# Kernel optimization log

Measured on AMD Instinct MI355X. Metric: run time of the kernel, lower is better.

The kernel has to match this reference:

```python
import jax, jax.numpy as jnp
import numpy as np

B, Q, C = 8, 100, 1024
H, W = 64, 64
NH = 16
HD = C // NH
SCALE = HD ** -0.5
LN_EPS = 1e-5


def setup_inputs() -> dict:
    key = jax.random.key(0)
    ks = jax.random.split(key, 8)
    xav = lambda k, shp: jax.random.normal(k, shp, jnp.float32) * (2.0 / (shp[0] + shp[-1])) ** 0.5
    return {
        "tgt": jax.random.normal(ks[0], (B, Q, C), jnp.float32),
        "memory": jax.random.normal(ks[1], (B, H, W, C), jnp.float32),
        "memory_pos_emb": jax.random.normal(ks[2], (B, H, W, C), jnp.float32),
        "query_pos_emb": jax.random.normal(ks[3], (B, Q, C), jnp.float32),
        "Wq": xav(ks[4], (C, C)),
        "Wk": xav(ks[5], (C, C)),
        "Wv": xav(ks[6], (C, C)),
        "Wo": xav(ks[7], (C, C)),
        "bo": jnp.zeros((C,), jnp.float32),
        "ln_gamma": jnp.ones((C,), jnp.float32),
        "ln_beta": jnp.zeros((C,), jnp.float32),
    }


def _layernorm(x, g, b):
    mu = jnp.mean(x, axis=-1, keepdims=True)
    var = jnp.var(x, axis=-1, keepdims=True)
    return (x - mu) * jax.lax.rsqrt(var + LN_EPS) * g + b


def reference(tgt, memory, memory_pos_emb, query_pos_emb, Wq, Wk, Wv, Wo, bo, ln_gamma, ln_beta):
    # flatten spatial dims: [B,H,W,C] -> [B,K,C]
    mem = memory.reshape(B, H * W, C)
    mpos = memory_pos_emb.reshape(B, H * W, C)
    q_in = tgt + query_pos_emb          # [B,Q,C]
    k_in = mem + mpos                    # [B,K,C]
    # projections (torch Linear: x @ W.T), split heads -> [B,nh,*,hd]
    q = (q_in @ Wq.T).reshape(B, Q, NH, HD).transpose(0, 2, 1, 3)
    k = (k_in @ Wk.T).reshape(B, -1, NH, HD).transpose(0, 2, 1, 3)
    v = (mem @ Wv.T).reshape(B, -1, NH, HD).transpose(0, 2, 1, 3)
    dots = jnp.einsum('bhid,bhjd->bhij', q, k) * SCALE   # [B,nh,Q,K]
    # slot attention: softmax over QUERY axis, then renormalize over keys
    attn = jax.nn.softmax(dots, axis=2)
    attn = attn / (jnp.sum(attn, axis=-1, keepdims=True) + 1e-8)
    updates = jnp.einsum('bhij,bhjd->bhid', attn, v)     # [B,nh,Q,hd]
    updates = updates.transpose(0, 2, 1, 3).reshape(B, Q, C)
    out = updates @ Wo.T + bo
    # residual (dropout is identity in eval) + post-LayerNorm
    return _layernorm(tgt + out, ln_gamma, ln_beta)
```

## Files before the change

### kernel.cpp

```cpp
#include <hip/hip_runtime.h>

typedef unsigned short u16;
typedef __attribute__((ext_vector_type(8))) short bf16x8;
typedef __attribute__((ext_vector_type(4))) short bf16x4;
typedef __attribute__((ext_vector_type(4))) float f32x4;
typedef __attribute__((ext_vector_type(4))) unsigned short u16x4;
typedef __attribute__((ext_vector_type(8))) unsigned short u16x8;
typedef __attribute__((ext_vector_type(4))) int i32x4;
typedef __attribute__((ext_vector_type(4))) float f4;

#define DI __device__ __forceinline__


DI u16 f2bf(float f){
  unsigned int u = __float_as_uint(f);
  return (u16)((u + 0x7FFFu + ((u >> 16) & 1u)) >> 16);
}

DI void gl_lds16(const void* g, void* l){
  __builtin_amdgcn_global_load_lds((const __attribute__((address_space(1))) unsigned int*)g,
                                   (__attribute__((address_space(3))) unsigned int*)l, 16, 0, 0);
}

__global__ __launch_bounds__(256) void prep_kv(const float* __restrict__ mem,
                                               const float* __restrict__ mpos,
                                               u16* __restrict__ kA, u16* __restrict__ vA){
  const int t = blockIdx.x * 256 + threadIdx.x;
  #pragma unroll
  for (int i = 0; i < 2; ++i){
    const size_t g = (size_t)t + (size_t)i * 2097152;
    f4 m0 = ((const f4*)mem)[g * 2];
    f4 m1 = ((const f4*)mem)[g * 2 + 1];
    f4 p0 = ((const f4*)mpos)[g * 2];
    f4 p1 = ((const f4*)mpos)[g * 2 + 1];
    u16x8 k, v;
    #pragma unroll
    for (int j = 0; j < 4; ++j){
      k[j]     = f2bf(m0[j] + p0[j]);  v[j]     = f2bf(m0[j]);
      k[j + 4] = f2bf(m1[j] + p1[j]);  v[j + 4] = f2bf(m1[j]);
    }
    ((u16x8*)kA)[g] = k;
    ((u16x8*)vA)[g] = v;
  }
}

__global__ __launch_bounds__(256) void prep_qw(const float* __restrict__ tgt,
                                               const float* __restrict__ qpos,
                                               const float* __restrict__ Wq, const float* __restrict__ Wk,
                                               const float* __restrict__ Wv, const float* __restrict__ Wo,
                                               u16* __restrict__ qA, u16* __restrict__ Wbf){
  int gid = blockIdx.x * 256 + threadIdx.x;
  const int NQ4 = 819200 / 4;
  if (gid < NQ4){
    f4 a = ((const f4*)tgt)[gid];
    f4 b = ((const f4*)qpos)[gid];
    u16x4 r;
    #pragma unroll
    for (int j = 0; j < 4; ++j) r[j] = f2bf(a[j] + b[j]);
    ((u16x4*)qA)[gid] = r;
  } else {
    int wid = gid - NQ4;
    int sel = wid >> 18;
    int off = wid & 262143;
    const float* W = (sel == 0) ? Wq : (sel == 1) ? Wk : (sel == 2) ? Wv : Wo;
    f4 w = ((const f4*)W)[off];
    u16x4 r;
    #pragma unroll
    for (int j = 0; j < 4; ++j) r[j] = f2bf(w[j]);
    ((u16x4*)(Wbf))[(size_t)sel * 262144 + off] = r;
  }
}

__global__ __launch_bounds__(512, 1) void gemm256(
    const u16* __restrict__ A, const u16* __restrict__ Bw,
    u16* __restrict__ Cb, float scale)
{
  __shared__ __align__(16) char lds[131072];
  const int tid = threadIdx.x;
  const int l = tid & 63, w = tid >> 6;
  const int nwg = gridDim.x;
  const int sbid = (blockIdx.x & 7) * (nwg >> 3) + (blockIdx.x >> 3);
  const int mb = sbid >> 2, nb = sbid & 3;
  const int m0 = mb * 256, n0 = nb * 256;
  const int fr = l & 15, fg = l >> 4;
  const int wm = w >> 2, wn = w & 3;

  char* ldsA  = lds + wm * 8192 + l * 16;
  char* ldsB  = lds + 32768 + wn * 4096 + l * 16;
  char* ldsS0 = lds + w * 1024;
  char* ldsS1 = lds + (8 + w) * 1024;
  const u16* gA0 = A  + (size_t)(m0 + w * 16 + fr) * 1024 + fg * 8;
  const u16* gA1 = A  + (size_t)(m0 + (8 + w) * 16 + fr) * 1024 + fg * 8;
  const u16* gB0 = Bw + (size_t)(n0 + w * 16 + fr) * 1024 + fg * 8;
  const u16* gB1 = Bw + (size_t)(n0 + (8 + w) * 16 + fr) * 1024 + fg * 8;

  auto stA = [&](int pp, int kh, int kt){
    const int o = kt * 64 + kh * 32;
    gl_lds16(gA0 + o, ldsS0 + pp * 65536 + kh * 16384);
    gl_lds16(gA1 + o, ldsS1 + pp * 65536 + kh * 16384);
  };
  auto stB = [&](int pp, int kh, int kt){
    const int o = kt * 64 + kh * 32;
    gl_lds16(gB0 + o, ldsS0 + pp * 65536 + 32768 + kh * 16384);
    gl_lds16(gB1 + o, ldsS1 + pp * 65536 + 32768 + kh * 16384);
  };
  auto rdA4 = [&](bf16x8* av, int pp, int kh, int mfb){
    #pragma unroll
    for (int i = 0; i < 4; ++i)
      av[i] = *(const bf16x8*)(ldsA + pp * 65536 + kh * 16384 + (mfb + i) * 1024);
  };
  auto rdB4 = [&](bf16x8* bv, int pp, int kh){
    #pragma unroll
    for (int i = 0; i < 4; ++i)
      bv[i] = *(const bf16x8*)(ldsB + pp * 65536 + kh * 16384 + i * 1024);
  };

  f32x4 acc[8][4] = {};

  stA(0, 0, 0); stB(0, 0, 0); stA(0, 1, 0); stB(0, 1, 0);
  stA(1, 0, 1); stB(1, 0, 1);
  asm volatile("s_waitcnt vmcnt(8)" ::: "memory");
  __builtin_amdgcn_s_barrier();

  auto ktbody = [&](int P, int kt){
    const int kt1 = (kt + 1 > 15) ? 15 : kt + 1;
    const int kt2 = (kt + 2 > 15) ? 15 : kt + 2;
    bf16x8 av[4], bv[4];

    rdA4(av, P, 0, 0); rdB4(bv, P, 0);
    stA(P ^ 1, 1, kt1);
    __builtin_amdgcn_s_barrier();
    __builtin_amdgcn_s_setprio(1);
    #pragma unroll
    for (int i = 0; i < 4; ++i)
      #pragma unroll
      for (int n = 0; n < 4; ++n)
        acc[i][n] = __builtin_amdgcn_mfma_f32_16x16x32_bf16(av[i], bv[n], acc[i][n], 0, 0, 0);
    __builtin_amdgcn_s_setprio(0);
    __builtin_amdgcn_s_barrier();

    rdA4(av, P, 0, 4);
    stB(P ^ 1, 1, kt1);
    asm volatile("s_waitcnt vmcnt(8)" ::: "memory");
    __builtin_amdgcn_s_barrier();
    __builtin_amdgcn_s_setprio(1);
    #pragma unroll
    for (int i = 0; i < 4; ++i)
      #pragma unroll
      for (int n = 0; n < 4; ++n)
        acc[4 + i][n] = __builtin_amdgcn_mfma_f32_16x16x32_bf16(av[i], bv[n], acc[4 + i][n], 0, 0, 0);
    __builtin_amdgcn_s_setprio(0);
    __builtin_amdgcn_s_barrier();

    rdA4(av, P, 1, 0); rdB4(bv, P, 1);
    stA(P, 0, kt2);
    __builtin_amdgcn_s_barrier();
    __builtin_amdgcn_s_setprio(1);
    #pragma unroll
    for (int i = 0; i < 4; ++i)
      #pragma unroll
      for (int n = 0; n < 4; ++n)
        acc[i][n] = __builtin_amdgcn_mfma_f32_16x16x32_bf16(av[i], bv[n], acc[i][n], 0, 0, 0);
    __builtin_amdgcn_s_setprio(0);
    __builtin_amdgcn_s_barrier();

    rdA4(av, P, 1, 4);
    stB(P, 0, kt2);
    asm volatile("s_waitcnt vmcnt(8)" ::: "memory");
    __builtin_amdgcn_s_barrier();
    __builtin_amdgcn_s_setprio(1);
    #pragma unroll
    for (int i = 0; i < 4; ++i)
      #pragma unroll
      for (int n = 0; n < 4; ++n)
        acc[4 + i][n] = __builtin_amdgcn_mfma_f32_16x16x32_bf16(av[i], bv[n], acc[4 + i][n], 0, 0, 0);
    __builtin_amdgcn_s_setprio(0);
    __builtin_amdgcn_s_barrier();
  };

  for (int kk = 0; kk < 8; ++kk){
    ktbody(0, 2 * kk);
    ktbody(1, 2 * kk + 1);
  }

  asm volatile("s_waitcnt vmcnt(0)" ::: "memory");

  #pragma unroll
  for (int mf = 0; mf < 8; ++mf){
    #pragma unroll
    for (int nf = 0; nf < 4; ++nf){
      const int gcol = n0 + wn * 64 + nf * 16 + fr;
      #pragma unroll
      for (int r = 0; r < 4; ++r){
        const int grow = m0 + wm * 128 + mf * 16 + fg * 4 + r;
        Cb[(size_t)grow * 1024 + gcol] = f2bf(acc[mf][nf][r] * scale);
      }
    }
  }
}

template<int MODE>
__global__ __launch_bounds__(256, 2) void gemm_bt(
    const u16* __restrict__ A, const u16* __restrict__ Bw,
    u16* __restrict__ Cb, float* __restrict__ Cf,
    const float* __restrict__ bias, const float* __restrict__ resid,
    int M, float scale)
{
  __shared__ u16 lA[2][128 * 32];
  __shared__ u16 lB[2][128 * 32];
  const int tid = threadIdx.x;
  const int l = tid & 63, w = tid >> 6;
  const int nwg = gridDim.x;
  int bid = blockIdx.x;
  bid = (bid & 7) * (nwg >> 3) + (bid >> 3);
  const int mb = bid >> 3, nb = bid & 7;
  const int m0 = mb * 128, n0 = nb * 128;
  const int fr = l & 15, fg = l >> 4;
  const int wr = w >> 1, wc = w & 1;

  f32x4 acc[4][4] = {};

  auto stage = [&](int buf, int kt){
    const int k0 = kt * 32;
    #pragma unroll
    for (int q = 0; q < 2; ++q){
      int r = w * 32 + q * 16 + (l >> 2);
      int ar = m0 + r; if (ar >= M) ar = M - 1;
      gl_lds16(A  + (size_t)ar * 1024 + k0 + (l & 3) * 8, &lA[buf][(w * 32 + q * 16) * 32]);
      gl_lds16(Bw + (size_t)(n0 + r) * 1024 + k0 + (l & 3) * 8, &lB[buf][(w * 32 + q * 16) * 32]);
    }
  };

  stage(0, 0);
  __syncthreads();
  for (int kt = 0; kt < 32; ++kt){
    const int cur = kt & 1;
    if (kt < 31) stage(cur ^ 1, kt + 1);
    bf16x8 av[4], bv[4];
    #pragma unroll
    for (int m = 0; m < 4; ++m)
      av[m] = *(const bf16x8*)&lA[cur][(wr * 64 + m * 16 + fr) * 32 + fg * 8];
    #pragma unroll
    for (int n = 0; n < 4; ++n)
      bv[n] = *(const bf16x8*)&lB[cur][(wc * 64 + n * 16 + fr) * 32 + fg * 8];
    #pragma unroll
    for (int m = 0; m < 4; ++m)
      #pragma unroll
      for (int n = 0; n < 4; ++n)
        acc[m][n] = __builtin_amdgcn_mfma_f32_16x16x32_bf16(av[m], bv[n], acc[m][n], 0, 0, 0);
    __syncthreads();
  }

  #pragma unroll
  for (int m = 0; m < 4; ++m){
    const int grow_base = m0 + wr * 64 + m * 16 + fg * 4;
    #pragma unroll
    for (int n = 0; n < 4; ++n){
      const int gcol = n0 + wc * 64 + n * 16 + fr;
      #pragma unroll
      for (int r = 0; r < 4; ++r){
        const int grow = grow_base + r;
        if (grow < M){
          const float v = acc[m][n][r];
          if (MODE == 0) Cb[(size_t)grow * 1024 + gcol] = f2bf(v * scale);
          else           Cf[(size_t)grow * 1024 + gcol] = v + bias[gcol] + resid[(size_t)grow * 1024 + gcol];
        }
      }
    }
  }
}

__global__ __launch_bounds__(64, 1) void attn_k(
    const u16* __restrict__ qp, const u16* __restrict__ kp, const u16* __restrict__ vp,
    float* __restrict__ updpart, float* __restrict__ rspart)
{
  const int bidx = blockIdx.x;
  const int c = bidx & 7, h = (bidx >> 3) & 15, b = bidx >> 7;
  const int bh = b * 16 + h;
  const int l = threadIdx.x;
  const int fr = l & 15, fg = l >> 4;

  __shared__ u16 qlds[112 * 64];
  for (int t = 0; t < 14; ++t){
    int chunk = t * 64 + l;
    int row = chunk >> 3, cb = chunk & 7;
    i32x4 val = {0, 0, 0, 0};
    if (row < 100)
      val = *(const i32x4*)(qp + (size_t)(b * 100 + row) * 1024 + h * 64 + cb * 8);
    *(i32x4*)((char*)qlds + row * 128 + ((cb ^ (row & 7)) * 16)) = val;
  }
  __syncthreads();

  bf16x8 qf[7][2];
  #pragma unroll
  for (int n = 0; n < 7; ++n)
    #pragma unroll
    for (int ks = 0; ks < 2; ++ks){
      int row = n * 16 + fr;
      int cb = ks * 4 + fg;
      qf[n][ks] = *(const bf16x8*)((const char*)qlds + row * 128 + ((cb ^ (row & 7)) * 16));
    }

  f32x4 acc[7][4] = {};
  float rs[7] = {};
  const f32x4 fz = {0.f, 0.f, 0.f, 0.f};
  const size_t kvbase = ((size_t)b * 4096) * 1024 + h * 64;

  for (int t = 0; t < 32; ++t){
    const int j0 = c * 512 + t * 16;
    bf16x8 kf0 = *(const bf16x8*)(kp + kvbase + (size_t)(j0 + fr) * 1024 + fg * 8);
    bf16x8 kf1 = *(const bf16x8*)(kp + kvbase + (size_t)(j0 + fr) * 1024 + 32 + fg * 8);
    f32x4 s[7];
    #pragma unroll
    for (int n = 0; n < 7; ++n){
      s[n] = __builtin_amdgcn_mfma_f32_16x16x32_bf16(kf0, qf[n][0], fz, 0, 0, 0);
      s[n] = __builtin_amdgcn_mfma_f32_16x16x32_bf16(kf1, qf[n][1], s[n], 0, 0, 0);
    }
    if (fr >= 4){ s[6][0] = -1e30f; s[6][1] = -1e30f; s[6][2] = -1e30f; s[6][3] = -1e30f; }

    float pv[7][4];
    #pragma unroll
    for (int r = 0; r < 4; ++r){
      float m = s[0][r];
      #pragma unroll
      for (int n = 1; n < 7; ++n) m = fmaxf(m, s[n][r]);
      m = fmaxf(m, __shfl_xor(m, 1)); m = fmaxf(m, __shfl_xor(m, 2));
      m = fmaxf(m, __shfl_xor(m, 4)); m = fmaxf(m, __shfl_xor(m, 8));
      float sum = 0.f;
      #pragma unroll
      for (int n = 0; n < 7; ++n){ float e = __expf(s[n][r] - m); pv[n][r] = e; sum += e; }
      sum += __shfl_xor(sum, 1); sum += __shfl_xor(sum, 2);
      sum += __shfl_xor(sum, 4); sum += __shfl_xor(sum, 8);
      float inv = 1.0f / sum;
      #pragma unroll
      for (int n = 0; n < 7; ++n) pv[n][r] *= inv;
    }

    bf16x4 pk[7];
    #pragma unroll
    for (int n = 0; n < 7; ++n){
      rs[n] += pv[n][0] + pv[n][1] + pv[n][2] + pv[n][3];
      bf16x4 t4;
      t4[0] = (short)f2bf(pv[n][0]); t4[1] = (short)f2bf(pv[n][1]);
      t4[2] = (short)f2bf(pv[n][2]); t4[3] = (short)f2bf(pv[n][3]);
      pk[n] = t4;
    }

    bf16x4 vf[4];
    #pragma unroll
    for (int dt = 0; dt < 4; ++dt){
      bf16x4 tv;
      #pragma unroll
      for (int jj = 0; jj < 4; ++jj)
        tv[jj] = (short)vp[kvbase + (size_t)(j0 + fg * 4 + jj) * 1024 + dt * 16 + fr];
      vf[dt] = tv;
    }

    #pragma unroll
    for (int n = 0; n < 7; ++n)
      #pragma unroll
      for (int dt = 0; dt < 4; ++dt)
        acc[n][dt] = __builtin_amdgcn_mfma_f32_16x16x16bf16_1k(vf[dt], pk[n], acc[n][dt], 0, 0, 0);
  }

  #pragma unroll
  for (int n = 0; n < 7; ++n){
    float v = rs[n];
    v += __shfl_xor(v, 16); v += __shfl_xor(v, 32);
    if (l < 16) rspart[((size_t)c * 128 + bh) * 112 + n * 16 + l] = v;
  }
  float* ub = updpart + ((size_t)c * 128 + bh) * 64 * 112;
  #pragma unroll
  for (int n = 0; n < 7; ++n)
    #pragma unroll
    for (int dt = 0; dt < 4; ++dt)
      #pragma unroll
      for (int r = 0; r < 4; ++r){
        int d = dt * 16 + fg * 4 + r;
        int i = n * 16 + fr;
        ub[d * 112 + i] = acc[n][dt][r];
      }
}

__global__ __launch_bounds__(256) void nrm_k(const float* __restrict__ updpart,
                                             const float* __restrict__ rspart,
                                             u16* __restrict__ updn){
  int gid = blockIdx.x * 256 + threadIdx.x;
  int b = gid / 102400;
  int rem = gid % 102400;
  int i = rem / 1024;
  int cc = rem & 1023;
  int h = cc >> 6, d = cc & 63;
  int bh = b * 16 + h;
  float sum = 0.f, rsum = 0.f;
  #pragma unroll
  for (int c = 0; c < 8; ++c){
    sum  += updpart[(((size_t)c * 128 + bh) * 64 + d) * 112 + i];
    rsum += rspart[((size_t)c * 128 + bh) * 112 + i];
  }
  updn[gid] = f2bf(sum / (rsum + 1e-8f));
}

__global__ __launch_bounds__(256) void ln_k(const float* __restrict__ x,
                                            const float* __restrict__ g,
                                            const float* __restrict__ be,
                                            float* __restrict__ out){
  const int row = blockIdx.x;
  const int tid = threadIdx.x;
  const f4 xv = *(const f4*)(x + (size_t)row * 1024 + tid * 4);
  float s = xv[0] + xv[1] + xv[2] + xv[3];
  float q = xv[0]*xv[0] + xv[1]*xv[1] + xv[2]*xv[2] + xv[3]*xv[3];
  #pragma unroll
  for (int m = 1; m < 64; m <<= 1){ s += __shfl_xor(s, m); q += __shfl_xor(q, m); }
  __shared__ float ss[4], qq[4];
  const int w = tid >> 6;
  if ((tid & 63) == 0){ ss[w] = s; qq[w] = q; }
  __syncthreads();
  s = ss[0] + ss[1] + ss[2] + ss[3];
  q = qq[0] + qq[1] + qq[2] + qq[3];
  const float mu = s * (1.0f / 1024.0f);
  const float var = q * (1.0f / 1024.0f) - mu * mu;
  const float rstd = rsqrtf(var + 1e-5f);
  const f4 gv = *(const f4*)(g + tid * 4);
  const f4 bv = *(const f4*)(be + tid * 4);
  f4 o;
  #pragma unroll
  for (int j = 0; j < 4; ++j) o[j] = (xv[j] - mu) * rstd * gv[j] + bv[j];
  *(f4*)(out + (size_t)row * 1024 + tid * 4) = o;
}

extern "C" void kernel_launch(void* const* d_in, const int* in_sizes, int n_in,
                              void* d_out, int out_size, void* d_ws, size_t ws_size,
                              hipStream_t stream)
{
  const float* tgt   = (const float*)d_in[0];
  const float* mem   = (const float*)d_in[1];
  const float* mpos  = (const float*)d_in[2];
  const float* qpos  = (const float*)d_in[3];
  const float* Wq    = (const float*)d_in[4];
  const float* Wk    = (const float*)d_in[5];
  const float* Wv    = (const float*)d_in[6];
  const float* Wo    = (const float*)d_in[7];
  const float* bo    = (const float*)d_in[8];
  const float* gamma = (const float*)d_in[9];
  const float* beta  = (const float*)d_in[10];

  char* ws = (char*)d_ws;
  u16* qA     = (u16*)(ws + 0);
  u16* Wbf    = (u16*)(ws + 1638400);
  u16* kA     = (u16*)(ws + 10027008);
  u16* vA     = (u16*)(ws + 77135872);
  u16* qproj  = (u16*)(ws + 144244736);
  u16* kproj  = (u16*)(ws + 145883136);
  u16* vproj  = kA;
  float* updpart = (float*)(ws + 77135872);
  float* rspart  = (float*)(ws + 77135872 + 29360128);
  u16*   updn    = (u16*)  (ws + 77135872 + 29818880);
  float* resid   = (float*)(ws + 77135872 + 31457280);

  prep_kv<<<8192, 256, 0, stream>>>(mem, mpos, kA, vA);
  prep_qw<<<4896, 256, 0, stream>>>(tgt, qpos, Wq, Wk, Wv, Wo, qA, Wbf);
  gemm_bt<0><<<56,  256, 0, stream>>>(qA, Wbf, qproj, nullptr, nullptr, nullptr, 800, 0.125f);
  gemm256<<<512, 512, 0, stream>>>(kA, Wbf + 1048576, kproj, 1.0f);
  gemm256<<<512, 512, 0, stream>>>(vA, Wbf + 2097152, vproj, 1.0f);
  attn_k<<<1024, 64, 0, stream>>>(qproj, kproj, vproj, updpart, rspart);
  nrm_k<<<3200, 256, 0, stream>>>(updpart, rspart, updn);
  gemm_bt<1><<<56, 256, 0, stream>>>(updn, Wbf + 3145728, nullptr, resid, bo, tgt, 800, 1.0f);
  ln_k<<<800, 256, 0, stream>>>(resid, gamma, beta, (float*)d_out);
}
```

Measured before the change: 402.0 us.

## Use 4-wave 256x256 GEMM with 128x128 warp tiles; nontemporal prep loads

The K/V projection GEMM now runs with 4 waves per block instead of 8. Each wave computes a 128x128 output sub-tile with 64 accumulators and issues four global-to-LDS loads per stage, which raises MFMA work per LDS read and reduces barrier participants. The cost is much higher register pressure and less latency hiding per CU. The K/V prep kernel also processes four chunks per thread with nontemporal loads and half the blocks, to cut cache pollution and launch overhead on the large streaming input.

```diff
diff --git a/kernel.cpp b/kernel.cpp
--- a/kernel.cpp
+++ b/kernel.cpp
@@ -27,12 +27,12 @@
                                                u16* __restrict__ kA, u16* __restrict__ vA){
   const int t = blockIdx.x * 256 + threadIdx.x;
   #pragma unroll
-  for (int i = 0; i < 2; ++i){
-    const size_t g = (size_t)t + (size_t)i * 2097152;
-    f4 m0 = ((const f4*)mem)[g * 2];
-    f4 m1 = ((const f4*)mem)[g * 2 + 1];
-    f4 p0 = ((const f4*)mpos)[g * 2];
-    f4 p1 = ((const f4*)mpos)[g * 2 + 1];
+  for (int i = 0; i < 4; ++i){
+    const size_t g = (size_t)t + (size_t)i * 1048576;
+    f4 m0 = __builtin_nontemporal_load((const f4*)mem  + g * 2);
+    f4 m1 = __builtin_nontemporal_load((const f4*)mem  + g * 2 + 1);
+    f4 p0 = __builtin_nontemporal_load((const f4*)mpos + g * 2);
+    f4 p1 = __builtin_nontemporal_load((const f4*)mpos + g * 2 + 1);
     u16x8 k, v;
     #pragma unroll
     for (int j = 0; j < 4; ++j){
@@ -71,7 +71,7 @@
   }
 }
 
-__global__ __launch_bounds__(512, 1) void gemm256(
+__global__ __launch_bounds__(256, 1) void gemm256(
     const u16* __restrict__ A, const u16* __restrict__ Bw,
     u16* __restrict__ Cb, float scale)
 {
@@ -83,97 +83,96 @@
   const int mb = sbid >> 2, nb = sbid & 3;
   const int m0 = mb * 256, n0 = nb * 256;
   const int fr = l & 15, fg = l >> 4;
-  const int wm = w >> 2, wn = w & 3;
-
-  char* ldsA  = lds + wm * 8192 + l * 16;
-  char* ldsB  = lds + 32768 + wn * 4096 + l * 16;
-  char* ldsS0 = lds + w * 1024;
-  char* ldsS1 = lds + (8 + w) * 1024;
-  const u16* gA0 = A  + (size_t)(m0 + w * 16 + fr) * 1024 + fg * 8;
-  const u16* gA1 = A  + (size_t)(m0 + (8 + w) * 16 + fr) * 1024 + fg * 8;
-  const u16* gB0 = Bw + (size_t)(n0 + w * 16 + fr) * 1024 + fg * 8;
-  const u16* gB1 = Bw + (size_t)(n0 + (8 + w) * 16 + fr) * 1024 + fg * 8;
+  const int wm = w >> 1, wn = w & 1;
+
+  char* ldsA = lds + wm * 8192 + l * 16;
+  char* ldsB = lds + 32768 + wn * 8192 + l * 16;
+  char* ldsS = lds + w * 1024;
+  const u16* gA = A  + (size_t)(m0 + w * 16 + fr) * 1024 + fg * 8;
+  const u16* gB = Bw + (size_t)(n0 + w * 16 + fr) * 1024 + fg * 8;
 
   auto stA = [&](int pp, int kh, int kt){
     const int o = kt * 64 + kh * 32;
-    gl_lds16(gA0 + o, ldsS0 + pp * 65536 + kh * 16384);
-    gl_lds16(gA1 + o, ldsS1 + pp * 65536 + kh * 16384);
+    #pragma unroll
+    for (int q = 0; q < 4; ++q)
+      gl_lds16(gA + q * 65536 + o, ldsS + pp * 65536 + kh * 16384 + q * 4096);
   };
   auto stB = [&](int pp, int kh, int kt){
     const int o = kt * 64 + kh * 32;
-    gl_lds16(gB0 + o, ldsS0 + pp * 65536 + 32768 + kh * 16384);
-    gl_lds16(gB1 + o, ldsS1 + pp * 65536 + 32768 + kh * 16384);
-  };
-  auto rdA4 = [&](bf16x8* av, int pp, int kh, int mfb){
+    #pragma unroll
+    for (int q = 0; q < 4; ++q)
+      gl_lds16(gB + q * 65536 + o, ldsS + pp * 65536 + 32768 + kh * 16384 + q * 4096);
+  };
+  auto rdA8 = [&](bf16x8* av, int pp, int kh){
+    #pragma unroll
+    for (int i = 0; i < 8; ++i)
+      av[i] = *(const bf16x8*)(ldsA + pp * 65536 + kh * 16384 + i * 1024);
+  };
+  auto rdB4 = [&](bf16x8* bv, int pp, int kh, int nfb){
     #pragma unroll
     for (int i = 0; i < 4; ++i)
-      av[i] = *(const bf16x8*)(ldsA + pp * 65536 + kh * 16384 + (mfb + i) * 1024);
-  };
-  auto rdB4 = [&](bf16x8* bv, int pp, int kh){
-    #pragma unroll
-    for (int i = 0; i < 4; ++i)
-      bv[i] = *(const bf16x8*)(ldsB + pp * 65536 + kh * 16384 + i * 1024);
-  };
-
-  f32x4 acc[8][4] = {};
+      bv[i] = *(const bf16x8*)(ldsB + pp * 65536 + kh * 16384 + (nfb + i) * 1024);
+  };
+
+  f32x4 acc[8][8] = {};
 
   stA(0, 0, 0); stB(0, 0, 0); stA(0, 1, 0); stB(0, 1, 0);
   stA(1, 0, 1); stB(1, 0, 1);
-  asm volatile("s_waitcnt vmcnt(8)" ::: "memory");
+  asm volatile("s_waitcnt vmcnt(16)" ::: "memory");
   __builtin_amdgcn_s_barrier();
 
   auto ktbody = [&](int P, int kt){
     const int kt1 = (kt + 1 > 15) ? 15 : kt + 1;
     const int kt2 = (kt + 2 > 15) ? 15 : kt + 2;
-    bf16x8 av[4], bv[4];
-
-    rdA4(av, P, 0, 0); rdB4(bv, P, 0);
+    bf16x8 av[8], bv[4];
+
+    rdA8(av, P, 0); rdB4(bv, P, 0, 0);
     stA(P ^ 1, 1, kt1);
     __builtin_amdgcn_s_barrier();
     __builtin_amdgcn_s_setprio(1);
     #pragma unroll
-    for (int i = 0; i < 4; ++i)
+    for (int mf = 0; mf < 8; ++mf)
       #pragma unroll
       for (int n = 0; n < 4; ++n)
-        acc[i][n] = __builtin_amdgcn_mfma_f32_16x16x32_bf16(av[i], bv[n], acc[i][n], 0, 0, 0);
+        acc[mf][n] = __builtin_amdgcn_mfma_f32_16x16x32_bf16(av[mf], bv[n], acc[mf][n], 0, 0, 0);
     __builtin_amdgcn_s_setprio(0);
     __builtin_amdgcn_s_barrier();
 
-    rdA4(av, P, 0, 4);
+    rdB4(bv, P, 0, 4);
     stB(P ^ 1, 1, kt1);
-    asm volatile("s_waitcnt vmcnt(8)" ::: "memory");
+    asm volatile("s_waitcnt vmcnt(16)" ::: "memory");
     __builtin_amdgcn_s_barrier();
     __builtin_amdgcn_s_setprio(1);
     #pragma unroll
-    for (int i = 0; i < 4; ++i)
+    for (int mf = 0; mf < 8; ++mf)
       #pragma unroll
       for (int n = 0; n < 4; ++n)
-        acc[4 + i][n] = __builtin_amdgcn_mfma_f32_16x16x32_bf16(av[i], bv[n], acc[4 + i][n], 0, 0, 0);
+        acc[mf][4 + n] = __builtin_amdgcn_mfma_f32_16x16x32_bf16(av[mf], bv[n], acc[mf][4 + n], 0, 0, 0);
     __builtin_amdgcn_s_setprio(0);
     __builtin_amdgcn_s_barrier();
 
-    rdA4(av, P, 1, 0); rdB4(bv, P, 1);
+    rdA8(av, P, 1); rdB4(bv, P, 1, 0);
     stA(P, 0, kt2);
     __builtin_amdgcn_s_barrier();
     __builtin_amdgcn_s_setprio(1);
     #pragma unroll
-    for (int i = 0; i < 4; ++i)
+    for (int mf = 0; mf < 8; ++mf)
       #pragma unroll
       for (int n = 0; n < 4; ++n)
-        acc[i][n] = __builtin_amdgcn_mfma_f32_16x16x32_bf16(av[i], bv[n], acc[i][n], 0, 0, 0);
+        acc[mf][n] = __builtin_amdgcn_mfma_f32_16x16x32_bf16(av[mf], bv[n], acc[mf][n], 0, 0, 0);
     __builtin_amdgcn_s_setprio(0);
     __builtin_amdgcn_s_barrier();
 
-    rdA4(av, P, 1, 4);
+    rdB4(bv, P, 1, 4);
     stB(P, 0, kt2);
-    asm volatile("s_waitcnt vmcnt(8)" ::: "memory");
+    asm volatile("s_waitcnt vmcnt(16)" ::: "memory");
     __builtin_amdgcn_s_barrier();
     __builtin_amdgcn_s_setprio(1);
     #pragma unroll
-    for (int i = 0; i < 4; ++i)
+    for (int mf = 0; mf < 8; ++mf)
       #pragma unroll
       for (int n = 0; n < 4; ++n)
-        acc[4 + i][n] = __builtin_amdgcn_mfma_f32_16x16x32_bf16(av[i], bv[n], acc[4 + i][n], 0, 0, 0);
+        acc[mf][4 + n] = __builtin_amdgcn_mfma_f32_16x16x32_bf16(av[mf], bv[n], acc[mf][4 + n], 0, 0, 0);
     __builtin_amdgcn_s_setprio(0);
     __builtin_amdgcn_s_barrier();
   };
@@ -188,8 +187,8 @@
   #pragma unroll
   for (int mf = 0; mf < 8; ++mf){
     #pragma unroll
-    for (int nf = 0; nf < 4; ++nf){
-      const int gcol = n0 + wn * 64 + nf * 16 + fr;
+    for (int nf = 0; nf < 8; ++nf){
+      const int gcol = n0 + wn * 128 + nf * 16 + fr;
       #pragma unroll
       for (int r = 0; r < 4; ++r){
         const int grow = m0 + wm * 128 + mf * 16 + fg * 4 + r;
@@ -458,11 +457,11 @@
   u16*   updn    = (u16*)  (ws + 77135872 + 29818880);
   float* resid   = (float*)(ws + 77135872 + 31457280);
 
-  prep_kv<<<8192, 256, 0, stream>>>(mem, mpos, kA, vA);
+  prep_kv<<<4096, 256, 0, stream>>>(mem, mpos, kA, vA);
   prep_qw<<<4896, 256, 0, stream>>>(tgt, qpos, Wq, Wk, Wv, Wo, qA, Wbf);
   gemm_bt<0><<<56,  256, 0, stream>>>(qA, Wbf, qproj, nullptr, nullptr, nullptr, 800, 0.125f);
-  gemm256<<<512, 512, 0, stream>>>(kA, Wbf + 1048576, kproj, 1.0f);
-  gemm256<<<512, 512, 0, stream>>>(vA, Wbf + 2097152, vproj, 1.0f);
+  gemm256<<<512, 256, 0, stream>>>(kA, Wbf + 1048576, kproj, 1.0f);
+  gemm256<<<512, 256, 0, stream>>>(vA, Wbf + 2097152, vproj, 1.0f);
   attn_k<<<1024, 64, 0, stream>>>(qproj, kproj, vproj, updpart, rspart);
   nrm_k<<<3200, 256, 0, stream>>>(updpart, rspart, updn);
   gemm_bt<1><<<56, 256, 0, stream>>>(updn, Wbf + 3145728, nullptr, resid, bo, tgt, 800, 1.0f);
```

After: 481.4 us. 1.2x slower.
